# Optimization experiments

Hardware: AMD Instinct MI355X
Metric: run time of the kernel (lower is better)

Reference implementation:

```python
import jax, jax.numpy as jnp
import numpy as np

B, S, E = 4, 2048, 1024


def setup_inputs() -> dict:
    key = jax.random.key(0)
    ks = jax.random.split(key, 7)
    sc = 1.0 / np.sqrt(E)
    return {
        "embedded": jax.random.normal(ks[0], (B, S, E), dtype=jnp.float32),
        "Wk": jax.random.normal(ks[1], (E, E), dtype=jnp.float32) * sc,
        "bk": jax.random.normal(ks[2], (E,), dtype=jnp.float32) * 0.01,
        "Wq": jax.random.normal(ks[3], (E, E), dtype=jnp.float32) * sc,
        "bq": jax.random.normal(ks[4], (E,), dtype=jnp.float32) * 0.01,
        "Wv": jax.random.normal(ks[5], (E, E), dtype=jnp.float32) * sc,
        "bv": jax.random.normal(ks[6], (E,), dtype=jnp.float32) * 0.01,
    }


def reference(embedded, Wk, bk, Wq, bq, Wv, bv):
    # embedded: [B, S, E]
    K = embedded @ Wk.T + bk  # [B,S,E]
    Q = embedded @ Wq.T + bq
    V = embedded @ Wv.T + bv
    seq_len = K.shape[1]
    # score[b,i,j] = K_i . Q_j, scaled by 1/sqrt(seq_len) (as in original)
    scores = jnp.einsum('bie,bje->bij', K, Q) / jnp.sqrt(jnp.asarray(seq_len, K.dtype))
    # softmax over dim=-2 -> over the key index i
    W = jax.nn.softmax(scores, axis=-2)  # [B,S,S]
    # Y = (V^T @ W)^T -> Y[b,j,d] = sum_i V[b,i,d] * W[b,i,j]
    Y = jnp.einsum('bid,bij->bjd', V, W)  # [B,S,E]
    return Y
```

## Files before the change

### kernel.cpp

```cpp
#include <hip/hip_runtime.h>
#include <hip/hip_bf16.h>


typedef __bf16 bf16x8 __attribute__((ext_vector_type(8)));
typedef float  f32x4  __attribute__((ext_vector_type(4)));

__device__ __forceinline__ unsigned short f2bf(float f) {
    unsigned int u = __float_as_uint(f);
    u = (u + 0x7FFFu + ((u >> 16) & 1u)) >> 16;
    return (unsigned short)u;
}

__global__ __launch_bounds__(256)
void cvt_all(const float* __restrict__ X,  const float* __restrict__ Wq,
             const float* __restrict__ Wk, const float* __restrict__ Wv,
             unsigned short* __restrict__ Xb,  unsigned short* __restrict__ Wqb,
             unsigned short* __restrict__ Wkb, unsigned short* __restrict__ Wvb,
             float* __restrict__ l) {
    long i = (long)blockIdx.x * 256 + threadIdx.x;
    if (i < 8192) l[i] = 0.0f;
    const float* src; unsigned short* dst; long off;
    if (i < 2097152L) { src = X; dst = Xb; off = i; }
    else {
        long j = i - 2097152L;
        int w = (int)(j >> 18);
        off = j & 262143L;
        src = (w == 0) ? Wq : (w == 1) ? Wk : Wv;
        dst = (w == 0) ? Wqb : (w == 1) ? Wkb : Wvb;
    }
    float4 v = reinterpret_cast<const float4*>(src)[off];
    ushort4 o;
    o.x = f2bf(v.x); o.y = f2bf(v.y); o.z = f2bf(v.z); o.w = f2bf(v.w);
    reinterpret_cast<ushort4*>(dst)[off] = o;
}

#define GEMM_DECLS                                                      \
    const int t    = threadIdx.x;                                       \
    const int wave = t >> 6;                                            \
    const int lane = t & 63;                                            \
    const int quad = lane >> 4;                                         \
    const int lr   = lane & 15;                                         \
    const int wm   = (wave >> 1) * 64;                                  \
    const int wn   = (wave & 1) * 64;                                   \
    const int sx   = lr & 7;                                            \
    const int lrow = lane >> 3;                                         \
    const int gch  = ((lane & 7) ^ (lrow & 7)) * 8;

#define GEMM_KLOOP(Aptr, Bptr, LDA, LDB)                                \
    for (int k0 = 0; k0 < K; k0 += 64) {                                \
        _Pragma("unroll")                                               \
        for (int r = 0; r < 4; ++r) {                                   \
            const int rowb = wave * 8 + r * 32;                         \
            const int row  = rowb + lrow;                               \
            const long goffA = (long)(m0 + row) * (LDA) + k0 + gch;     \
            const long goffB = (long)(n0 + row) * (LDB) + k0 + gch;     \
            __builtin_amdgcn_global_load_lds(                           \
                (const __attribute__((address_space(1))) void*)((Aptr) + goffA), \
                (__attribute__((address_space(3))) void*)(&lsA[rowb * 64]), 16, 0, 0); \
            __builtin_amdgcn_global_load_lds(                           \
                (const __attribute__((address_space(1))) void*)((Bptr) + goffB), \
                (__attribute__((address_space(3))) void*)(&lsB[rowb * 64]), 16, 0, 0); \
        }                                                               \
        __syncthreads();                                                \
        _Pragma("unroll")                                               \
        for (int h = 0; h < 2; ++h) {                                   \
            const int cp = ((h * 4 + quad) ^ sx) * 8;                   \
            bf16x8 af[4], bfr[4];                                       \
            _Pragma("unroll")                                           \
            for (int i = 0; i < 4; ++i) {                               \
                af[i]  = __builtin_bit_cast(bf16x8,                     \
                          *reinterpret_cast<const uint4*>(&lsA[(wm + i * 16 + lr) * 64 + cp])); \
                bfr[i] = __builtin_bit_cast(bf16x8,                     \
                          *reinterpret_cast<const uint4*>(&lsB[(wn + i * 16 + lr) * 64 + cp])); \
            }                                                           \
            _Pragma("unroll")                                           \
            for (int i = 0; i < 4; ++i)                                 \
                _Pragma("unroll")                                       \
                for (int j = 0; j < 4; ++j)                             \
                    acc[i][j] = __builtin_amdgcn_mfma_f32_16x16x32_bf16(af[i], bfr[j], acc[i][j], 0, 0, 0); \
        }                                                               \
        __syncthreads();                                                \
    }

__global__ __launch_bounds__(256, 2)
void gemm_qkv(const unsigned short* __restrict__ Xb,
              const unsigned short* __restrict__ Wqb,
              const unsigned short* __restrict__ Wkb,
              const unsigned short* __restrict__ Wvb,
              const float* __restrict__ bq, const float* __restrict__ bk,
              const float* __restrict__ bv_,
              unsigned short* __restrict__ Qb, unsigned short* __restrict__ Kb,
              unsigned short* __restrict__ Vt)
{
    __shared__ unsigned short lsA[128 * 64];
    __shared__ unsigned short lsB[128 * 64];

    const int id  = blockIdx.x;
    const int g   = id & 7;
    const int jj  = id >> 3;
    const int xx  = jj & 7;
    const int yin = (jj >> 3) & 7;
    const int z   = jj >> 6;

    const unsigned short* A = Xb;
    const unsigned short* B = (z == 0) ? Wqb : (z == 1) ? Wkb : Wvb;
    const float* bias       = (z == 0) ? bq  : (z == 1) ? bk  : bv_;

    const int n0 = xx * 128;
    const int m0 = (g * 8 + yin) * 128;
    const int K = 1024;

    GEMM_DECLS
    f32x4 acc[4][4] = {};
    GEMM_KLOOP(A, B, 1024, 1024)

#pragma unroll
    for (int j = 0; j < 4; ++j) {
        const int n = n0 + wn + j * 16 + lr;
        const float bvv = bias[n];
#pragma unroll
        for (int i = 0; i < 4; ++i) {
            const int mbase = m0 + wm + i * 16 + quad * 4;
            if (z < 2) {
                unsigned short* C = (z == 0) ? Qb : Kb;
#pragma unroll
                for (int r = 0; r < 4; ++r)
                    C[(long)(mbase + r) * 1024 + n] = f2bf(acc[i][j][r] + bvv);
            } else {
                ushort4 o;
                o.x = f2bf(acc[i][j][0] + bvv);
                o.y = f2bf(acc[i][j][1] + bvv);
                o.z = f2bf(acc[i][j][2] + bvv);
                o.w = f2bf(acc[i][j][3] + bvv);
                long boff = (long)(mbase >> 11) * (1024L * 2048) + (long)n * 2048 + (mbase & 2047);
                *reinterpret_cast<ushort4*>(Vt + boff) = o;
            }
        }
    }
}

__global__ __launch_bounds__(256, 2)
void gemm_scores(const unsigned short* __restrict__ Q,
                 const unsigned short* __restrict__ Kp,
                 unsigned short* __restrict__ P, float* __restrict__ l,
                 float scale)
{
    __shared__ unsigned short lsA[128 * 64];
    __shared__ unsigned short lsB[128 * 64];

    const int id  = blockIdx.x;
    const int g   = id & 7;
    const int u   = id >> 3;
    const int bz  = g >> 1;
    const int mh  = g & 1;
    const int xx  = u & 15;
    const int yin = u >> 4;

    const unsigned short* A = Q  + (long)bz * 2048 * 1024;
    const unsigned short* B = Kp + (long)bz * 2048 * 1024;
    unsigned short* Pb = P + (long)bz * 2048 * 2048;
    float* lb = l + bz * 2048;

    const int n0 = xx * 128;
    const int m0 = (mh * 8 + yin) * 128;
    const int K = 1024;

    GEMM_DECLS
    f32x4 acc[4][4] = {};
    GEMM_KLOOP(A, B, 1024, 1024)

#pragma unroll
    for (int i = 0; i < 4; ++i) {
#pragma unroll
        for (int r = 0; r < 4; ++r) {
            const int m = m0 + wm + i * 16 + quad * 4 + r;
            float psum = 0.0f;
#pragma unroll
            for (int j = 0; j < 4; ++j) {
                const float p = __expf(acc[i][j][r] * scale);
                psum += p;
                const int n = n0 + wn + j * 16 + lr;
                Pb[(long)m * 2048 + n] = f2bf(p);
            }
#pragma unroll
            for (int o = 1; o < 16; o <<= 1) psum += __shfl_xor(psum, o, 64);
            if (lr == 0) atomicAdd(&lb[m], psum);
        }
    }
}

__global__ __launch_bounds__(256, 2)
void gemm_y(const unsigned short* __restrict__ P,
            const unsigned short* __restrict__ Vt,
            const float* __restrict__ l, float* __restrict__ out)
{
    __shared__ unsigned short lsA[128 * 64];
    __shared__ unsigned short lsB[128 * 64];

    const int id  = blockIdx.x;
    const int g   = id & 7;
    const int u   = id >> 3;
    const int bz  = g >> 1;
    const int mh  = g & 1;
    const int xx  = u & 7;
    const int yin = u >> 3;

    const unsigned short* A = P  + (long)bz * 2048 * 2048;
    const unsigned short* B = Vt + (long)bz * 1024 * 2048;
    const float* lb = l + bz * 2048;
    float* C = out + (long)bz * 2048 * 1024;

    const int n0 = xx * 128;
    const int m0 = (mh * 8 + yin) * 128;
    const int K = 2048;

    GEMM_DECLS
    f32x4 acc[4][4] = {};
    GEMM_KLOOP(A, B, 2048, 2048)

    float linv[4][4];
#pragma unroll
    for (int i = 0; i < 4; ++i)
#pragma unroll
        for (int r = 0; r < 4; ++r)
            linv[i][r] = 1.0f / lb[m0 + wm + i * 16 + quad * 4 + r];

#pragma unroll
    for (int j = 0; j < 4; ++j) {
        const int n = n0 + wn + j * 16 + lr;
#pragma unroll
        for (int i = 0; i < 4; ++i) {
            const int mbase = m0 + wm + i * 16 + quad * 4;
#pragma unroll
            for (int r = 0; r < 4; ++r)
                C[(long)(mbase + r) * 1024 + n] = acc[i][j][r] * linv[i][r];
        }
    }
}

extern "C" void kernel_launch(void* const* d_in, const int* in_sizes, int n_in,
                              void* d_out, int out_size, void* d_ws, size_t ws_size,
                              hipStream_t stream) {
    const float* X  = (const float*)d_in[0];
    const float* Wk = (const float*)d_in[1];
    const float* bk = (const float*)d_in[2];
    const float* Wq = (const float*)d_in[3];
    const float* bq = (const float*)d_in[4];
    const float* Wv = (const float*)d_in[5];
    const float* bv = (const float*)d_in[6];
    float* out = (float*)d_out;

    const size_t MB = 1024 * 1024;
    if (ws_size < 80 * MB) return;

    char* ws = (char*)d_ws;
    unsigned short* Vt  = (unsigned short*)(ws);
    unsigned short* P   = (unsigned short*)(ws + 16 * MB);
    unsigned short* Xbf = (unsigned short*)(ws + 16 * MB);
    float*          l   = (float*)(ws + 48 * MB);
    unsigned short* Wqb = (unsigned short*)(ws + 49 * MB);
    unsigned short* Wkb = (unsigned short*)(ws + 51 * MB);
    unsigned short* Wvb = (unsigned short*)(ws + 53 * MB);
    unsigned short* Qb = (unsigned short*)d_out;
    unsigned short* Kb = Qb + 8192L * 1024;

    dim3 blk(256);

    cvt_all<<<2883584 / 256, blk, 0, stream>>>(X, Wq, Wk, Wv, Xbf, Wqb, Wkb, Wvb, l);

    gemm_qkv<<<1536, blk, 0, stream>>>(Xbf, Wqb, Wkb, Wvb, bq, bk, bv, Qb, Kb, Vt);

    gemm_scores<<<1024, blk, 0, stream>>>(Qb, Kb, P, l, 0.022097086912079608f);

    gemm_y<<<512, blk, 0, stream>>>(P, Vt, l, out);
}
```

Measured before the change: 231.0 us.

## Fold Wk^T·Wq into one matrix to skip separate Q and K projections

The K·Q scores are rewritten as X·(Wk^T Wq)·X^T plus rank-one bias terms. A small precomputed 1024x1024 matrix M replaces the separate Q and K GEMMs, and the bias contributions u, w and a constant are added in the softmax epilogue. This removes one of the three large projection GEMMs. In exchange it adds an extra weight-sized GEMM, transpose conversion of Wq and Wk, and small GEMV kernels, and it rounds M to bf16, which changes numerical error. The tile ordering in the scores and Y GEMMs is also swapped.

After: 415.5 us. 79.9% more time.

```diff
diff --git a/kernel.cpp b/kernel.cpp
--- a/kernel.cpp
+++ b/kernel.cpp
@@ -11,27 +11,68 @@
     return (unsigned short)u;
 }
 
+__device__ __forceinline__ float wave_reduce(float s) {
+#pragma unroll
+    for (int o = 32; o; o >>= 1) s += __shfl_xor(s, o, 64);
+    return s;
+}
+
+__device__ __forceinline__ float dot8(uint4 xv, float4 a, float4 b) {
+    bf16x8 x = __builtin_bit_cast(bf16x8, xv);
+    return (float)x[0]*a.x + (float)x[1]*a.y + (float)x[2]*a.z + (float)x[3]*a.w
+         + (float)x[4]*b.x + (float)x[5]*b.y + (float)x[6]*b.z + (float)x[7]*b.w;
+}
+
 __global__ __launch_bounds__(256)
 void cvt_all(const float* __restrict__ X,  const float* __restrict__ Wq,
              const float* __restrict__ Wk, const float* __restrict__ Wv,
-             unsigned short* __restrict__ Xb,  unsigned short* __restrict__ Wqb,
-             unsigned short* __restrict__ Wkb, unsigned short* __restrict__ Wvb,
+             unsigned short* __restrict__ Xb,  unsigned short* __restrict__ Wqt,
+             unsigned short* __restrict__ Wkt, unsigned short* __restrict__ Wvb,
              float* __restrict__ l) {
-    long i = (long)blockIdx.x * 256 + threadIdx.x;
-    if (i < 8192) l[i] = 0.0f;
-    const float* src; unsigned short* dst; long off;
-    if (i < 2097152L) { src = X; dst = Xb; off = i; }
-    else {
-        long j = i - 2097152L;
-        int w = (int)(j >> 18);
-        off = j & 262143L;
-        src = (w == 0) ? Wq : (w == 1) ? Wk : Wv;
-        dst = (w == 0) ? Wqb : (w == 1) ? Wkb : Wvb;
-    }
-    float4 v = reinterpret_cast<const float4*>(src)[off];
-    ushort4 o;
-    o.x = f2bf(v.x); o.y = f2bf(v.y); o.z = f2bf(v.z); o.w = f2bf(v.w);
-    reinterpret_cast<ushort4*>(dst)[off] = o;
+    __shared__ unsigned short tile[64 * 72];
+    const int blk = blockIdx.x;
+    const int t = threadIdx.x;
+
+    if (blk < 8192) {
+        long i = (long)blk * 256 + t;
+        if (i < 8192) l[i] = 0.0f;
+        float4 v = reinterpret_cast<const float4*>(X)[i];
+        ushort4 o; o.x = f2bf(v.x); o.y = f2bf(v.y); o.z = f2bf(v.z); o.w = f2bf(v.w);
+        reinterpret_cast<ushort4*>(Xb)[i] = o;
+    } else if (blk < 9216) {
+        long i = (long)(blk - 8192) * 256 + t;
+        float4 v = reinterpret_cast<const float4*>(Wv)[i];
+        ushort4 o; o.x = f2bf(v.x); o.y = f2bf(v.y); o.z = f2bf(v.z); o.w = f2bf(v.w);
+        reinterpret_cast<ushort4*>(Wvb)[i] = o;
+    } else {
+        const int tt  = blk - 9216;
+        const int mat = tt >> 8;
+        const int tl  = tt & 255;
+        const int tr  = tl >> 4;
+        const int tc  = tl & 15;
+        const float* src = mat ? Wk : Wq;
+        unsigned short* dst = mat ? Wkt : Wqt;
+        const int r  = t >> 2;
+        const int c4 = t & 3;
+#pragma unroll
+        for (int it = 0; it < 4; ++it) {
+            const int cc = c4 + it * 4;
+            float4 v = *reinterpret_cast<const float4*>(
+                src + (long)(tr * 64 + r) * 1024 + tc * 64 + cc * 4);
+            tile[(cc * 4 + 0) * 72 + r] = f2bf(v.x);
+            tile[(cc * 4 + 1) * 72 + r] = f2bf(v.y);
+            tile[(cc * 4 + 2) * 72 + r] = f2bf(v.z);
+            tile[(cc * 4 + 3) * 72 + r] = f2bf(v.w);
+        }
+        __syncthreads();
+        const int rp = t >> 2;
+#pragma unroll
+        for (int it = 0; it < 2; ++it) {
+            const int ch = (t & 3) + it * 4;
+            *reinterpret_cast<uint4*>(dst + (long)(tc * 64 + rp) * 1024 + tr * 64 + ch * 8)
+                = *reinterpret_cast<const uint4*>(&tile[rp * 72 + ch * 8]);
+        }
+    }
 }
 
 #define GEMM_DECLS                                                      \
@@ -83,49 +124,124 @@
     }
 
 __global__ __launch_bounds__(256, 2)
-void gemm_qkv(const unsigned short* __restrict__ Xb,
-              const unsigned short* __restrict__ Wqb,
-              const unsigned short* __restrict__ Wkb,
-              const unsigned short* __restrict__ Wvb,
-              const float* __restrict__ bq, const float* __restrict__ bk,
-              const float* __restrict__ bv_,
-              unsigned short* __restrict__ Qb, unsigned short* __restrict__ Kb,
-              unsigned short* __restrict__ Vt)
+void aux_k(const unsigned short* __restrict__ Wkt,
+           const unsigned short* __restrict__ Wqt,
+           const float* __restrict__ bq, const float* __restrict__ bk,
+           unsigned short* __restrict__ Mt,
+           float* __restrict__ g1, float* __restrict__ g2,
+           float* __restrict__ cbuf)
 {
     __shared__ unsigned short lsA[128 * 64];
     __shared__ unsigned short lsB[128 * 64];
-
-    const int id  = blockIdx.x;
+    const int blk = blockIdx.x;
+
+    if (blk < 64) {
+        const int m0 = (blk >> 3) * 128;
+        const int n0 = (blk & 7) * 128;
+        const int K = 1024;
+        GEMM_DECLS
+        f32x4 acc[4][4] = {};
+        GEMM_KLOOP(Wkt, Wqt, 1024, 1024)
+#pragma unroll
+        for (int j = 0; j < 4; ++j) {
+            const int n = n0 + wn + j * 16 + lr;
+#pragma unroll
+            for (int i = 0; i < 4; ++i) {
+                const int mbase = m0 + wm + i * 16 + quad * 4;
+#pragma unroll
+                for (int r = 0; r < 4; ++r)
+                    Mt[(long)(mbase + r) * 1024 + n] = f2bf(acc[i][j][r]);
+            }
+        }
+        return;
+    }
+
+    const int t = threadIdx.x;
+    const int wv = t >> 6, ln = t & 63;
+    const unsigned short* W = (blk == 64) ? Wqt : Wkt;
+    const float* bvec       = (blk == 64) ? bk  : bq;
+    float* gout             = (blk == 64) ? g1  : g2;
+    const float4* bf = reinterpret_cast<const float4*>(bvec);
+    float4 p0 = bf[ln * 2], p1 = bf[ln * 2 + 1];
+    float4 p2 = bf[128 + ln * 2], p3 = bf[128 + ln * 2 + 1];
+    for (int rr = 0; rr < 256; ++rr) {
+        const int e = wv * 256 + rr;
+        uint4 x0 = *reinterpret_cast<const uint4*>(W + (long)e * 1024 + ln * 8);
+        uint4 x1 = *reinterpret_cast<const uint4*>(W + (long)e * 1024 + 512 + ln * 8);
+        float s = wave_reduce(dot8(x0, p0, p1) + dot8(x1, p2, p3));
+        if (ln == 0) gout[e] = s;
+    }
+    if (blk == 65 && wv == 0) {
+        float s = 0.f;
+        for (int a = ln; a < 1024; a += 64) s += bq[a] * bk[a];
+        s = wave_reduce(s);
+        if (ln == 0) *cbuf = s;
+    }
+}
+
+__global__ __launch_bounds__(256, 2)
+void gemm_tv(const unsigned short* __restrict__ Xb,
+             const unsigned short* __restrict__ Mt,
+             const unsigned short* __restrict__ Wvb,
+             const float* __restrict__ bv_,
+             const float* __restrict__ g1, const float* __restrict__ g2,
+             const float* __restrict__ cbuf,
+             unsigned short* __restrict__ T, unsigned short* __restrict__ Vt,
+             float* __restrict__ u, float* __restrict__ w)
+{
+    __shared__ unsigned short lsA[128 * 64];
+    __shared__ unsigned short lsB[128 * 64];
+    const int id = blockIdx.x;
+
+    if (id >= 1024) {
+        const int t = threadIdx.x;
+        const int wave = t >> 6, lane = t & 63;
+        const int wid = (id - 1024) * 4 + wave;
+        const float* g = (wid < 64) ? g1 : g2;
+        const float4* gf = reinterpret_cast<const float4*>(g);
+        float4 q0 = gf[lane * 2], q1 = gf[lane * 2 + 1];
+        float4 q2 = gf[128 + lane * 2], q3 = gf[128 + lane * 2 + 1];
+        const float cadd = (wid < 64) ? 0.0f : *cbuf;
+        for (int rr = 0; rr < 128; ++rr) {
+            const int row  = wid * 128 + rr;
+            const int xrow = row & 8191;
+            uint4 x0 = *reinterpret_cast<const uint4*>(Xb + (long)xrow * 1024 + lane * 8);
+            uint4 x1 = *reinterpret_cast<const uint4*>(Xb + (long)xrow * 1024 + 512 + lane * 8);
+            float s = wave_reduce(dot8(x0, q0, q1) + dot8(x1, q2, q3));
+            if (lane == 0) {
+                if (row < 8192) u[row] = s;
+                else            w[row - 8192] = s + cadd;
+            }
+        }
+        return;
+    }
+
     const int g   = id & 7;
     const int jj  = id >> 3;
     const int xx  = jj & 7;
     const int yin = (jj >> 3) & 7;
     const int z   = jj >> 6;
 
-    const unsigned short* A = Xb;
-    const unsigned short* B = (z == 0) ? Wqb : (z == 1) ? Wkb : Wvb;
-    const float* bias       = (z == 0) ? bq  : (z == 1) ? bk  : bv_;
-
+    const unsigned short* B = (z == 0) ? Mt : Wvb;
     const int n0 = xx * 128;
     const int m0 = (g * 8 + yin) * 128;
     const int K = 1024;
 
     GEMM_DECLS
     f32x4 acc[4][4] = {};
-    GEMM_KLOOP(A, B, 1024, 1024)
+    GEMM_KLOOP(Xb, B, 1024, 1024)
 
 #pragma unroll
     for (int j = 0; j < 4; ++j) {
         const int n = n0 + wn + j * 16 + lr;
-        const float bvv = bias[n];
+        const float bvv = (z == 1) ? bv_[n] : 0.0f;
 #pragma unroll
         for (int i = 0; i < 4; ++i) {
             const int mbase = m0 + wm + i * 16 + quad * 4;
-            if (z < 2) {
-                unsigned short* C = (z == 0) ? Qb : Kb;
+            if (z == 0) {
 #pragma unroll
                 for (int r = 0; r < 4; ++r)
-                    C[(long)(mbase + r) * 1024 + n] = f2bf(acc[i][j][r] + bvv);
+                    T[(long)(mbase + r) * 1024 + n] = f2bf(acc[i][j][r]);
             } else {
                 ushort4 o;
                 o.x = f2bf(acc[i][j][0] + bvv);
@@ -140,8 +256,9 @@
 }
 
 __global__ __launch_bounds__(256, 2)
-void gemm_scores(const unsigned short* __restrict__ Q,
-                 const unsigned short* __restrict__ Kp,
+void gemm_scores(const unsigned short* __restrict__ T,
+                 const unsigned short* __restrict__ Xb,
+                 const float* __restrict__ u, const float* __restrict__ w,
                  unsigned short* __restrict__ P, float* __restrict__ l,
                  float scale)
 {
@@ -150,14 +267,14 @@
 
     const int id  = blockIdx.x;
     const int g   = id & 7;
-    const int u   = id >> 3;
+    const int uu  = id >> 3;
     const int bz  = g >> 1;
     const int mh  = g & 1;
-    const int xx  = u & 15;
-    const int yin = u >> 4;
-
-    const unsigned short* A = Q  + (long)bz * 2048 * 1024;
-    const unsigned short* B = Kp + (long)bz * 2048 * 1024;
+    const int yin = uu & 7;
+    const int xx  = uu >> 3;
+
+    const unsigned short* A = T  + (long)bz * 2048 * 1024;
+    const unsigned short* B = Xb + (long)bz * 2048 * 1024;
     unsigned short* Pb = P + (long)bz * 2048 * 2048;
     float* lb = l + bz * 2048;
 
@@ -169,15 +286,21 @@
     f32x4 acc[4][4] = {};
     GEMM_KLOOP(A, B, 1024, 1024)
 
+    float wn4[4];
+#pragma unroll
+    for (int j = 0; j < 4; ++j)
+        wn4[j] = w[bz * 2048 + n0 + wn + j * 16 + lr];
+
 #pragma unroll
     for (int i = 0; i < 4; ++i) {
 #pragma unroll
         for (int r = 0; r < 4; ++r) {
             const int m = m0 + wm + i * 16 + quad * 4 + r;
+            const float um = u[bz * 2048 + m];
             float psum = 0.0f;
 #pragma unroll
             for (int j = 0; j < 4; ++j) {
-                const float p = __expf(acc[i][j][r] * scale);
+                const float p = __expf((acc[i][j][r] + um + wn4[j]) * scale);
                 psum += p;
                 const int n = n0 + wn + j * 16 + lr;
                 Pb[(long)m * 2048 + n] = f2bf(p);
@@ -199,11 +322,11 @@
 
     const int id  = blockIdx.x;
     const int g   = id & 7;
-    const int u   = id >> 3;
+    const int uu  = id >> 3;
     const int bz  = g >> 1;
     const int mh  = g & 1;
-    const int xx  = u & 7;
-    const int yin = u >> 3;
+    const int yin = uu & 7;
+    const int xx  = uu >> 3;
 
     const unsigned short* A = P  + (long)bz * 2048 * 2048;
     const unsigned short* B = Vt + (long)bz * 1024 * 2048;
@@ -256,21 +379,28 @@
     char* ws = (char*)d_ws;
     unsigned short* Vt  = (unsigned short*)(ws);
     unsigned short* P   = (unsigned short*)(ws + 16 * MB);
-    unsigned short* Xbf = (unsigned short*)(ws + 16 * MB);
-    float*          l   = (float*)(ws + 48 * MB);
-    unsigned short* Wqb = (unsigned short*)(ws + 49 * MB);
-    unsigned short* Wkb = (unsigned short*)(ws + 51 * MB);
-    unsigned short* Wvb = (unsigned short*)(ws + 53 * MB);
-    unsigned short* Qb = (unsigned short*)d_out;
-    unsigned short* Kb = Qb + 8192L * 1024;
+    unsigned short* Xbf = (unsigned short*)(ws + 48 * MB);
+    unsigned short* Wqt = (unsigned short*)(ws + 64 * MB);
+    unsigned short* Wkt = (unsigned short*)(ws + 66 * MB);
+    unsigned short* Wvb = (unsigned short*)(ws + 68 * MB);
+    unsigned short* Mt  = (unsigned short*)(ws + 70 * MB);
+    float* l    = (float*)(ws + 72 * MB);
+    float* u    = (float*)(ws + 72 * MB + 32 * 1024);
+    float* w    = (float*)(ws + 72 * MB + 64 * 1024);
+    float* g1   = (float*)(ws + 72 * MB + 96 * 1024);
+    float* g2   = (float*)(ws + 72 * MB + 100 * 1024);
+    float* cbuf = (float*)(ws + 72 * MB + 104 * 1024);
+    unsigned short* T = (unsigned short*)d_out;
 
     dim3 blk(256);
 
-    cvt_all<<<2883584 / 256, blk, 0, stream>>>(X, Wq, Wk, Wv, Xbf, Wqb, Wkb, Wvb, l);
-
-    gemm_qkv<<<1536, blk, 0, stream>>>(Xbf, Wqb, Wkb, Wvb, bq, bk, bv, Qb, Kb, Vt);
-
-    gemm_scores<<<1024, blk, 0, stream>>>(Qb, Kb, P, l, 0.022097086912079608f);
+    cvt_all<<<9728, blk, 0, stream>>>(X, Wq, Wk, Wv, Xbf, Wqt, Wkt, Wvb, l);
+
+    aux_k<<<66, blk, 0, stream>>>(Wkt, Wqt, bq, bk, Mt, g1, g2, cbuf);
+
+    gemm_tv<<<1056, blk, 0, stream>>>(Xbf, Mt, Wvb, bv, g1, g2, cbuf, T, Vt, u, w);
+
+    gemm_scores<<<1024, blk, 0, stream>>>(T, Xbf, u, w, P, l, 0.022097086912079608f);
 
     gemm_y<<<512, blk, 0, stream>>>(P, Vt, l, out);
 }
```
